# Optimization experiments

Measured on AMD Instinct MI355X. Metric: run time of the kernel, lower is better.

## Reference

```python
import jax, jax.numpy as jnp
import numpy as np

B, C, D = 32, 8192, 256
TOPK = 512


def find_confounders(w, sample_w, k):
    # squared euclidean distance [B, C] = |s|^2 - 2 s.w^T + |w|^2
    dis = (sample_w ** 2).sum(axis=1, keepdims=True) - 2.0 * sample_w @ w.T + (w ** 2).sum(axis=1)[None, :]
    _, idx = jax.lax.top_k(-dis, k)  # k smallest distances
    return idx


def setup_inputs() -> dict:
    key = jax.random.key(0)
    k1, k2, k3, k4, k5 = jax.random.split(key, 5)
    weight = jax.random.normal(k1, (C, D), dtype=jnp.float32)
    mu = jax.random.normal(k2, (B, D), dtype=jnp.float32)
    # keep variance bounded away from 0 for numerical sanity
    var = jax.random.uniform(k3, (B, D), dtype=jnp.float32) * 0.9 + 0.1
    all_class_density = jax.random.uniform(k4, (B, C, D), dtype=jnp.float32)
    labels = jax.random.randint(k5, (B,), 0, C, dtype=jnp.int64)
    nontrivial = jnp.ones((B, C, D), dtype=bool)
    return {"weight": weight, "mu": mu, "var": var,
            "all_class_density": all_class_density,
            "labels": labels, "nontrivial": nontrivial}


def reference(weight, mu, var, all_class_density, labels, nontrivial):
    sample_weight = weight[labels]                                  # [B, D]
    diff = jax.lax.stop_gradient(sample_weight - mu)                # detached in torch
    density = jnp.exp(-diff ** 2 / (2.0 * var))                     # [B, D]
    total_density = jnp.clip(all_class_density.sum(axis=1), 1e-8)   # [B, D]

    # method == 1 branch: mask out the per-(b,d) argmin class from nontrivial
    argmin_idx = jnp.argmin(all_class_density, axis=1)              # [B, D]
    kill = jnp.arange(C)[None, :, None] == argmin_idx[:, None, :]   # [B, C, D]
    nt = nontrivial & ~kill
    minv = (all_class_density + (~nt) * 1000.0).min(axis=1, keepdims=True)  # [B,1,D]
    maxv = (all_class_density - nt * 1000.0).max(axis=1, keepdims=True)     # [B,1,D]
    overly = (nt & (minv - maxv >= 0.2 * total_density[:, None, :])).astype(jnp.float32)

    confid = density[:, None, :] / total_density[:, None, :] * (1.0 - overly)  # [B, C, D]

    # penalize: renormalize by density over top-512 nearest confounder classes
    topkidx = find_confounders(weight, sample_weight, TOPK)         # [B, K]
    topk_w = weight[topkidx]                                        # [B, K, D]
    acd_det = jnp.exp(-jax.lax.stop_gradient(topk_w - mu[:, None, :]) ** 2 / (2.0 * var[:, None, :]))
    total_det = jnp.clip(acd_det.sum(axis=1), 1e-8)                 # [B, D]
    confid = confid - density[:, None, :] / total_det[:, None, :] * overly

    return confid.mean(axis=-1).mean()
```

## Files before the change

### kernel.cpp

```cpp
#include <hip/hip_runtime.h>
#include <cfloat>
#include <cstddef>

#define B_ 32
#define C_ 8192
#define D_ 256
#define K_ 512
#define NCH 64
#define CPB (C_ / NCH)

typedef float f4n __attribute__((ext_vector_type(4)));

__global__ __launch_bounds__(256) void k1_colreduce(const float* __restrict__ acd,
                                                    float* __restrict__ psum,
                                                    float* __restrict__ pm1,
                                                    float* __restrict__ pm2,
                                                    unsigned* __restrict__ flag) {
    const int t = threadIdx.x;
    const int blk = blockIdx.x;
    if (blk == 0 && t == 0) *flag = 0u;
    const int b = blk / NCH, ch = blk % NCH;
    const int d4 = t & 63;
    const int coff = t >> 6;

    const f4n* src = (const f4n*)(acd + ((size_t)b * C_ + (size_t)ch * CPB) * D_);

    f4n s  = (f4n){0.f, 0.f, 0.f, 0.f};
    f4n m1 = (f4n){FLT_MAX, FLT_MAX, FLT_MAX, FLT_MAX};
    f4n m2 = m1;

#define UPD3(f) { s.f += x.f; float mx = fmaxf(m1.f, x.f); m2.f = fminf(m2.f, mx); m1.f = fminf(m1.f, x.f); }
#pragma unroll 4
    for (int r = coff; r < CPB; r += 4) {
        f4n x = __builtin_nontemporal_load(&src[(size_t)r * 64 + d4]);
        UPD3(x) UPD3(y) UPD3(z) UPD3(w)
    }
#undef UPD3

    __shared__ f4n ls[256];
    __shared__ f4n l1[256];
    __shared__ f4n l2[256];
    ls[t] = s; l1[t] = m1; l2[t] = m2;
    __syncthreads();

    if (t < 64) {
        f4n S = ls[t], M1 = l1[t], M2 = l2[t];
#define CMB(f) { S.f += s2.f; float mx = fmaxf(M1.f, a1.f); M2.f = fminf(fminf(M2.f, a2.f), mx); M1.f = fminf(M1.f, a1.f); }
#pragma unroll
        for (int j = 64; j < 256; j += 64) {
            f4n s2 = ls[t + j], a1 = l1[t + j], a2 = l2[t + j];
            CMB(x) CMB(y) CMB(z) CMB(w)
        }
#undef CMB
        size_t o = ((size_t)b * NCH + ch) * 64 + t;
        ((f4n*)psum)[o] = S;
        ((f4n*)pm1)[o] = M1;
        ((f4n*)pm2)[o] = M2;
    }
}

__global__ __launch_bounds__(256) void k2_finalize(const float* __restrict__ psum,
                                                   const float* __restrict__ pm1,
                                                   const float* __restrict__ pm2,
                                                   const float* __restrict__ weight,
                                                   const float* __restrict__ mu,
                                                   const float* __restrict__ var,
                                                   const int* __restrict__ labels,
                                                   float* __restrict__ dens_o,
                                                   float* __restrict__ tot_o,
                                                   float* __restrict__ ofl_o,
                                                   unsigned* __restrict__ flag) {
    const int b = blockIdx.x, d = threadIdx.x;
    float sum = 0.f, m1 = FLT_MAX, m2 = FLT_MAX;
    for (int ch = 0; ch < NCH; ch++) {
        size_t o = ((size_t)b * NCH + ch) * D_ + d;
        float cs = psum[o], c1 = pm1[o], c2 = pm2[o];
        sum += cs;
        m2 = fminf(fminf(m2, c2), fmaxf(m1, c1));
        m1 = fminf(m1, c1);
    }
    const int lab = labels[b];
    const float sw = weight[(size_t)lab * D_ + d];
    const float diff = sw - mu[b * D_ + d];
    const float v = var[b * D_ + d];
    const float dens = expf(-(diff * diff) / (2.0f * v));
    const float tot = fmaxf(sum, 1e-8f);
    const float o_ = (m2 - m1 >= 0.2f * tot) ? 1.0f : 0.0f;
    dens_o[b * D_ + d] = dens;
    tot_o[b * D_ + d] = tot;
    ofl_o[b * D_ + d] = o_;
    if (o_ != 0.0f) atomicOr(flag, 1u);
}

__device__ __forceinline__ unsigned fmapk(float f) {
    unsigned u = __float_as_uint(f);
    return (u & 0x80000000u) ? ~u : (u | 0x80000000u);
}

__global__ __launch_bounds__(256) void k345_det(const unsigned* __restrict__ flag,
                                                const float* __restrict__ weight,
                                                const float* __restrict__ mu,
                                                const float* __restrict__ var,
                                                const int* __restrict__ labels,
                                                float* __restrict__ total_det) {
    if (*flag == 0u) return;
    const int b = blockIdx.x, t = threadIdx.x;

    __shared__ unsigned kl[C_];
    __shared__ float s_s[D_];
    __shared__ unsigned hist[256];
    __shared__ unsigned scan[256];
    __shared__ int sel[K_];
    __shared__ unsigned sh_pref, sh_want, sh_nsel;

    s_s[t] = weight[(size_t)labels[b] * D_ + t];
    if (t == 0) { sh_pref = 0u; sh_want = K_; sh_nsel = 0u; }
    __syncthreads();

    for (int c = t; c < C_; c += 256) {
        const f4n* wr = (const f4n*)(weight + (size_t)c * D_);
        const f4n* sr = (const f4n*)s_s;
        float dot = 0.f, nsq = 0.f;
#pragma unroll 8
        for (int d4 = 0; d4 < D_ / 4; d4++) {
            f4n w = wr[d4], sv = sr[d4];
            dot += w.x * sv.x + w.y * sv.y + w.z * sv.z + w.w * sv.w;
            nsq += w.x * w.x + w.y * w.y + w.z * w.z + w.w * w.w;
        }
        kl[c] = fmapk(nsq - 2.0f * dot);
    }
    __syncthreads();

    for (int pass = 0; pass < 4; pass++) {
        const int shift = 24 - 8 * pass;
        hist[t] = 0u;
        __syncthreads();
        const unsigned pref = sh_pref;
        const unsigned pmask = (pass == 0) ? 0u : (0xFFFFFFFFu << (shift + 8));
        for (int c = t; c < C_; c += 256) {
            unsigned u = kl[c];
            if ((u & pmask) == (pref & pmask)) atomicAdd(&hist[(u >> shift) & 255u], 1u);
        }
        __syncthreads();
        unsigned h = hist[t];
        scan[t] = h;
        __syncthreads();
        for (int off = 1; off < 256; off <<= 1) {
            unsigned x = (t >= off) ? scan[t - off] : 0u;
            __syncthreads();
            scan[t] += x;
            __syncthreads();
        }
        const unsigned want = sh_want;
        const unsigned incl = scan[t], excl = incl - h;
        if (incl >= want && excl < want) {
            sh_pref = pref | ((unsigned)t << shift);
            sh_want = want - excl;
        }
        __syncthreads();
    }

    const unsigned Kk = sh_pref, quota = sh_want;
    for (int c = t; c < C_; c += 256) {
        unsigned u = kl[c];
        bool take = (u < Kk);
        if (!take && u == Kk) {
            unsigned r = 0;
            for (int j = 0; j < c; j++)
                if (kl[j] == Kk) r++;
            take = (r < quota);
        }
        if (take) {
            unsigned s = atomicAdd(&sh_nsel, 1u);
            sel[s] = c;
        }
    }
    __syncthreads();

    const float muv = mu[b * D_ + t];
    const float nh = -0.5f / var[b * D_ + t];
    float acc = 0.f;
    for (int k = 0; k < K_; k++) {
        float w = weight[(size_t)sel[k] * D_ + t];
        float df = w - muv;
        acc += expf(df * df * nh);
    }
    total_det[b * D_ + t] = acc;
}

__global__ __launch_bounds__(256) void k6_final(const float* __restrict__ dens,
                                                const float* __restrict__ tot,
                                                const float* __restrict__ ofl,
                                                const float* __restrict__ total_det,
                                                float* __restrict__ out) {
    const int t = threadIdx.x;
    double acc = 0.0;
    for (int i = t; i < B_ * D_; i += 256) {
        double dn = dens[i], tt = tot[i], o = ofl[i];
        acc += dn / tt * ((double)C_ - (double)(C_ - 1) * o);
        if (o != 0.0) {
            double td = fmax((double)total_det[i], 1e-8);
            acc -= dn / td * ((double)(C_ - 1) * o);
        }
    }
    __shared__ double red[256];
    red[t] = acc;
    __syncthreads();
    for (int s = 128; s > 0; s >>= 1) {
        if (t < s) red[t] += red[t + s];
        __syncthreads();
    }
    if (t == 0) out[0] = (float)(red[0] / ((double)B_ * (double)C_ * (double)D_));
}

extern "C" void kernel_launch(void* const* d_in, const int* in_sizes, int n_in,
                              void* d_out, int out_size, void* d_ws, size_t ws_size,
                              hipStream_t stream) {
    const float* weight = (const float*)d_in[0];
    const float* mu     = (const float*)d_in[1];
    const float* var    = (const float*)d_in[2];
    const float* acd    = (const float*)d_in[3];
    const int*   labels = (const int*)d_in[4];
    float* out = (float*)d_out;

    char* ws = (char*)d_ws;
    const size_t np = (size_t)B_ * NCH * D_;
    float* psum = (float*)ws;
    float* pm1  = psum + np;
    float* pm2  = pm1 + np;
    float* dens = pm2 + np;
    float* tot  = dens + B_ * D_;
    float* ofl  = tot + B_ * D_;
    float* tdet = ofl + B_ * D_;
    unsigned* flag = (unsigned*)(tdet + B_ * D_);

    k1_colreduce<<<B_ * NCH, 256, 0, stream>>>(acd, psum, pm1, pm2, flag);
    k2_finalize<<<B_, 256, 0, stream>>>(psum, pm1, pm2, weight, mu, var, labels,
                                        dens, tot, ofl, flag);
    k345_det<<<B_, 256, 0, stream>>>(flag, weight, mu, var, labels, tdet);
    k6_final<<<1, 256, 0, stream>>>(dens, tot, ofl, tdet, out);
}
```

Measured before the change: 462.1 us.

## Fuse finalize, top-k density and per-batch reduction into one kernel

Merges the finalize, confounder top-k/density and final-reduction kernels into one per-batch kernel. The kernel checks per block whether any overlap flag is set and only then runs the top-k selection, and writes a per-batch double partial that a tiny final kernel sums. The column-reduce chunk count is halved, giving fewer, longer blocks in the first pass and fewer partials to merge. This removes two launches and the intermediate global arrays. The cost is fewer blocks in the bandwidth-bound first pass and a large shared-memory footprint in the fused kernel.

```diff
diff --git a/kernel.cpp b/kernel.cpp
--- a/kernel.cpp
+++ b/kernel.cpp
@@ -6,7 +6,7 @@
 #define C_ 8192
 #define D_ 256
 #define K_ 512
-#define NCH 64
+#define NCH 32
 #define CPB (C_ / NCH)
 
 typedef float f4n __attribute__((ext_vector_type(4)));
@@ -14,12 +14,9 @@
 __global__ __launch_bounds__(256) void k1_colreduce(const float* __restrict__ acd,
                                                     float* __restrict__ psum,
                                                     float* __restrict__ pm1,
-                                                    float* __restrict__ pm2,
-                                                    unsigned* __restrict__ flag) {
+                                                    float* __restrict__ pm2) {
     const int t = threadIdx.x;
-    const int blk = blockIdx.x;
-    if (blk == 0 && t == 0) *flag = 0u;
-    const int b = blk / NCH, ch = blk % NCH;
+    const int b = blockIdx.x / NCH, ch = blockIdx.x % NCH;
     const int d4 = t & 63;
     const int coff = t >> 6;
 
@@ -59,158 +56,147 @@
     }
 }
 
-__global__ __launch_bounds__(256) void k2_finalize(const float* __restrict__ psum,
-                                                   const float* __restrict__ pm1,
-                                                   const float* __restrict__ pm2,
-                                                   const float* __restrict__ weight,
-                                                   const float* __restrict__ mu,
-                                                   const float* __restrict__ var,
-                                                   const int* __restrict__ labels,
-                                                   float* __restrict__ dens_o,
-                                                   float* __restrict__ tot_o,
-                                                   float* __restrict__ ofl_o,
-                                                   unsigned* __restrict__ flag) {
-    const int b = blockIdx.x, d = threadIdx.x;
+__device__ __forceinline__ unsigned fmapk(float f) {
+    unsigned u = __float_as_uint(f);
+    return (u & 0x80000000u) ? ~u : (u | 0x80000000u);
+}
+
+__global__ __launch_bounds__(256) void k2_fused(const float* __restrict__ psum,
+                                                const float* __restrict__ pm1,
+                                                const float* __restrict__ pm2,
+                                                const float* __restrict__ weight,
+                                                const float* __restrict__ mu,
+                                                const float* __restrict__ var,
+                                                const int* __restrict__ labels,
+                                                double* __restrict__ partial) {
+    const int b = blockIdx.x, t = threadIdx.x;
+
     float sum = 0.f, m1 = FLT_MAX, m2 = FLT_MAX;
     for (int ch = 0; ch < NCH; ch++) {
-        size_t o = ((size_t)b * NCH + ch) * D_ + d;
+        size_t o = ((size_t)b * NCH + ch) * D_ + t;
         float cs = psum[o], c1 = pm1[o], c2 = pm2[o];
         sum += cs;
         m2 = fminf(fminf(m2, c2), fmaxf(m1, c1));
         m1 = fminf(m1, c1);
     }
     const int lab = labels[b];
-    const float sw = weight[(size_t)lab * D_ + d];
-    const float diff = sw - mu[b * D_ + d];
-    const float v = var[b * D_ + d];
+    const float sw = weight[(size_t)lab * D_ + t];
+    const float muv = mu[b * D_ + t];
+    const float v = var[b * D_ + t];
+    const float diff = sw - muv;
     const float dens = expf(-(diff * diff) / (2.0f * v));
     const float tot = fmaxf(sum, 1e-8f);
     const float o_ = (m2 - m1 >= 0.2f * tot) ? 1.0f : 0.0f;
-    dens_o[b * D_ + d] = dens;
-    tot_o[b * D_ + d] = tot;
-    ofl_o[b * D_ + d] = o_;
-    if (o_ != 0.0f) atomicOr(flag, 1u);
-}
-
-__device__ __forceinline__ unsigned fmapk(float f) {
-    unsigned u = __float_as_uint(f);
-    return (u & 0x80000000u) ? ~u : (u | 0x80000000u);
-}
-
-__global__ __launch_bounds__(256) void k345_det(const unsigned* __restrict__ flag,
-                                                const float* __restrict__ weight,
-                                                const float* __restrict__ mu,
-                                                const float* __restrict__ var,
-                                                const int* __restrict__ labels,
-                                                float* __restrict__ total_det) {
-    if (*flag == 0u) return;
-    const int b = blockIdx.x, t = threadIdx.x;
-
-    __shared__ unsigned kl[C_];
-    __shared__ float s_s[D_];
-    __shared__ unsigned hist[256];
-    __shared__ unsigned scan[256];
-    __shared__ int sel[K_];
-    __shared__ unsigned sh_pref, sh_want, sh_nsel;
-
-    s_s[t] = weight[(size_t)labels[b] * D_ + t];
-    if (t == 0) { sh_pref = 0u; sh_want = K_; sh_nsel = 0u; }
-    __syncthreads();
-
-    for (int c = t; c < C_; c += 256) {
-        const f4n* wr = (const f4n*)(weight + (size_t)c * D_);
-        const f4n* sr = (const f4n*)s_s;
-        float dot = 0.f, nsq = 0.f;
+
+    double contrib = (double)dens / (double)tot *
+                     ((double)C_ - (double)(C_ - 1) * (double)o_);
+
+    __shared__ unsigned anyo;
+    if (t == 0) anyo = 0u;
+    __syncthreads();
+    if (o_ != 0.0f) atomicOr(&anyo, 1u);
+    __syncthreads();
+
+    if (anyo != 0u) {
+        __shared__ unsigned kl[C_];
+        __shared__ float s_s[D_];
+        __shared__ unsigned hist[256];
+        __shared__ unsigned scan[256];
+        __shared__ int sel[K_];
+        __shared__ unsigned sh_pref, sh_want, sh_nsel;
+
+        s_s[t] = sw;
+        if (t == 0) { sh_pref = 0u; sh_want = K_; sh_nsel = 0u; }
+        __syncthreads();
+
+        for (int c = t; c < C_; c += 256) {
+            const f4n* wr = (const f4n*)(weight + (size_t)c * D_);
+            const f4n* sr = (const f4n*)s_s;
+            float dot = 0.f, nsq = 0.f;
 #pragma unroll 8
-        for (int d4 = 0; d4 < D_ / 4; d4++) {
-            f4n w = wr[d4], sv = sr[d4];
-            dot += w.x * sv.x + w.y * sv.y + w.z * sv.z + w.w * sv.w;
-            nsq += w.x * w.x + w.y * w.y + w.z * w.z + w.w * w.w;
-        }
-        kl[c] = fmapk(nsq - 2.0f * dot);
-    }
-    __syncthreads();
-
-    for (int pass = 0; pass < 4; pass++) {
-        const int shift = 24 - 8 * pass;
-        hist[t] = 0u;
-        __syncthreads();
-        const unsigned pref = sh_pref;
-        const unsigned pmask = (pass == 0) ? 0u : (0xFFFFFFFFu << (shift + 8));
+            for (int d4 = 0; d4 < D_ / 4; d4++) {
+                f4n w = wr[d4], sv = sr[d4];
+                dot += w.x * sv.x + w.y * sv.y + w.z * sv.z + w.w * sv.w;
+                nsq += w.x * w.x + w.y * w.y + w.z * w.z + w.w * w.w;
+            }
+            kl[c] = fmapk(nsq - 2.0f * dot);
+        }
+        __syncthreads();
+
+        for (int pass = 0; pass < 4; pass++) {
+            const int shift = 24 - 8 * pass;
+            hist[t] = 0u;
+            __syncthreads();
+            const unsigned pref = sh_pref;
+            const unsigned pmask = (pass == 0) ? 0u : (0xFFFFFFFFu << (shift + 8));
+            for (int c = t; c < C_; c += 256) {
+                unsigned u = kl[c];
+                if ((u & pmask) == (pref & pmask)) atomicAdd(&hist[(u >> shift) & 255u], 1u);
+            }
+            __syncthreads();
+            unsigned h = hist[t];
+            scan[t] = h;
+            __syncthreads();
+            for (int off = 1; off < 256; off <<= 1) {
+                unsigned x = (t >= off) ? scan[t - off] : 0u;
+                __syncthreads();
+                scan[t] += x;
+                __syncthreads();
+            }
+            const unsigned want = sh_want;
+            const unsigned incl = scan[t], excl = incl - h;
+            if (incl >= want && excl < want) {
+                sh_pref = pref | ((unsigned)t << shift);
+                sh_want = want - excl;
+            }
+            __syncthreads();
+        }
+
+        const unsigned Kk = sh_pref, quota = sh_want;
         for (int c = t; c < C_; c += 256) {
             unsigned u = kl[c];
-            if ((u & pmask) == (pref & pmask)) atomicAdd(&hist[(u >> shift) & 255u], 1u);
-        }
-        __syncthreads();
-        unsigned h = hist[t];
-        scan[t] = h;
-        __syncthreads();
-        for (int off = 1; off < 256; off <<= 1) {
-            unsigned x = (t >= off) ? scan[t - off] : 0u;
-            __syncthreads();
-            scan[t] += x;
-            __syncthreads();
-        }
-        const unsigned want = sh_want;
-        const unsigned incl = scan[t], excl = incl - h;
-        if (incl >= want && excl < want) {
-            sh_pref = pref | ((unsigned)t << shift);
-            sh_want = want - excl;
-        }
-        __syncthreads();
-    }
-
-    const unsigned Kk = sh_pref, quota = sh_want;
-    for (int c = t; c < C_; c += 256) {
-        unsigned u = kl[c];
-        bool take = (u < Kk);
-        if (!take && u == Kk) {
-            unsigned r = 0;
-            for (int j = 0; j < c; j++)
-                if (kl[j] == Kk) r++;
-            take = (r < quota);
-        }
-        if (take) {
-            unsigned s = atomicAdd(&sh_nsel, 1u);
-            sel[s] = c;
-        }
-    }
-    __syncthreads();
-
-    const float muv = mu[b * D_ + t];
-    const float nh = -0.5f / var[b * D_ + t];
-    float acc = 0.f;
-    for (int k = 0; k < K_; k++) {
-        float w = weight[(size_t)sel[k] * D_ + t];
-        float df = w - muv;
-        acc += expf(df * df * nh);
-    }
-    total_det[b * D_ + t] = acc;
-}
-
-__global__ __launch_bounds__(256) void k6_final(const float* __restrict__ dens,
-                                                const float* __restrict__ tot,
-                                                const float* __restrict__ ofl,
-                                                const float* __restrict__ total_det,
-                                                float* __restrict__ out) {
+            bool take = (u < Kk);
+            if (!take && u == Kk) {
+                unsigned r = 0;
+                for (int j = 0; j < c; j++)
+                    if (kl[j] == Kk) r++;
+                take = (r < quota);
+            }
+            if (take) {
+                unsigned s2 = atomicAdd(&sh_nsel, 1u);
+                sel[s2] = c;
+            }
+        }
+        __syncthreads();
+
+        const float nh = -0.5f / v;
+        float acc = 0.f;
+        for (int k = 0; k < K_; k++) {
+            float w = weight[(size_t)sel[k] * D_ + t];
+            float df = w - muv;
+            acc += expf(df * df * nh);
+        }
+        double td = fmax((double)acc, 1e-8);
+        contrib -= (double)dens / td * (double)(C_ - 1) * (double)o_;
+    }
+
+    __shared__ double red[256];
+    red[t] = contrib;
+    __syncthreads();
+    for (int s2 = 128; s2 > 0; s2 >>= 1) {
+        if (t < s2) red[t] += red[t + s2];
+        __syncthreads();
+    }
+    if (t == 0) partial[b] = red[0];
+}
+
+__global__ __launch_bounds__(64) void k3_final(const double* __restrict__ partial,
+                                               float* __restrict__ out) {
     const int t = threadIdx.x;
-    double acc = 0.0;
-    for (int i = t; i < B_ * D_; i += 256) {
-        double dn = dens[i], tt = tot[i], o = ofl[i];
-        acc += dn / tt * ((double)C_ - (double)(C_ - 1) * o);
-        if (o != 0.0) {
-            double td = fmax((double)total_det[i], 1e-8);
-            acc -= dn / td * ((double)(C_ - 1) * o);
-        }
-    }
-    __shared__ double red[256];
-    red[t] = acc;
-    __syncthreads();
-    for (int s = 128; s > 0; s >>= 1) {
-        if (t < s) red[t] += red[t + s];
-        __syncthreads();
-    }
-    if (t == 0) out[0] = (float)(red[0] / ((double)B_ * (double)C_ * (double)D_));
+    double v = (t < B_) ? partial[t] : 0.0;
+#pragma unroll
+    for (int off = 32; off > 0; off >>= 1) v += __shfl_down(v, off);
+    if (t == 0) out[0] = (float)(v / ((double)B_ * (double)C_ * (double)D_));
 }
 
 extern "C" void kernel_launch(void* const* d_in, const int* in_sizes, int n_in,
@@ -228,15 +214,9 @@
     float* psum = (float*)ws;
     float* pm1  = psum + np;
     float* pm2  = pm1 + np;
-    float* dens = pm2 + np;
-    float* tot  = dens + B_ * D_;
-    float* ofl  = tot + B_ * D_;
-    float* tdet = ofl + B_ * D_;
-    unsigned* flag = (unsigned*)(tdet + B_ * D_);
-
-    k1_colreduce<<<B_ * NCH, 256, 0, stream>>>(acd, psum, pm1, pm2, flag);
-    k2_finalize<<<B_, 256, 0, stream>>>(psum, pm1, pm2, weight, mu, var, labels,
-                                        dens, tot, ofl, flag);
-    k345_det<<<B_, 256, 0, stream>>>(flag, weight, mu, var, labels, tdet);
-    k6_final<<<1, 256, 0, stream>>>(dens, tot, ofl, tdet, out);
-}
+    double* partial = (double*)(pm2 + np);
+
+    k1_colreduce<<<B_ * NCH, 256, 0, stream>>>(acd, psum, pm1, pm2);
+    k2_fused<<<B_, 256, 0, stream>>>(psum, pm1, pm2, weight, mu, var, labels, partial);
+    k3_final<<<1, 64, 0, stream>>>(partial, out);
+}
```

Measured after the change: 448.2 us. 3.0% less time.
